# Kernel tuning notes

Hardware: AMD Instinct MI355X
Metric: run time of the kernel (lower is better)

Reference implementation:

```python
import jax, jax.numpy as jnp
import numpy as np

EPS_BN = 1e-5


def conv2d(x, w, b, stride=1, pad=0):
    y = jax.lax.conv_general_dilated(
        x, w, (stride, stride), [(pad, pad), (pad, pad)],
        dimension_numbers=('NCHW', 'OIHW', 'NCHW'))
    return y + b[None, :, None, None]


def resize_ac(x, oh, ow):
    # bilinear resize, align_corners=True (matches F.interpolate(..., align_corners=True))
    N, C, H, W = x.shape
    ys = jnp.linspace(0.0, H - 1.0, oh)
    xs = jnp.linspace(0.0, W - 1.0, ow)
    y0 = jnp.floor(ys).astype(jnp.int32)
    x0 = jnp.floor(xs).astype(jnp.int32)
    y1 = jnp.minimum(y0 + 1, H - 1)
    x1 = jnp.minimum(x0 + 1, W - 1)
    wy = (ys - y0)[None, None, :, None]
    wx = (xs - x0)[None, None, None, :]
    top = jnp.take(x, y0, axis=2)
    bot = jnp.take(x, y1, axis=2)
    rows = top * (1.0 - wy) + bot * wy
    left = jnp.take(rows, x0, axis=3)
    right = jnp.take(rows, x1, axis=3)
    return left * (1.0 - wx) + right * wx


def grid_sample_3d(vol, grid):
    # vol: (N,C,D,H,W); grid: (N,Do,Ho,Wo,3) with channels (x->W, y->H, z->D)
    # trilinear, padding_mode='zeros', align_corners=False (torch defaults)
    N, C, D, H, W = vol.shape
    out_shape = grid.shape[1:4]
    gx = grid[..., 0].reshape(N, -1)
    gy = grid[..., 1].reshape(N, -1)
    gz = grid[..., 2].reshape(N, -1)
    ix = ((gx + 1.0) * W - 1.0) * 0.5
    iy = ((gy + 1.0) * H - 1.0) * 0.5
    iz = ((gz + 1.0) * D - 1.0) * 0.5
    x0 = jnp.floor(ix); y0 = jnp.floor(iy); z0 = jnp.floor(iz)
    fx = ix - x0; fy = iy - y0; fz = iz - z0
    volf = vol.reshape(N, C, D * H * W)

    def corner(xi, yi, zi, wgt):
        valid = ((xi >= 0) & (xi < W) & (yi >= 0) & (yi < H) & (zi >= 0) & (zi < D))
        xc = jnp.clip(xi, 0, W - 1).astype(jnp.int32)
        yc = jnp.clip(yi, 0, H - 1).astype(jnp.int32)
        zc = jnp.clip(zi, 0, D - 1).astype(jnp.int32)
        lin = (zc * H + yc) * W + xc  # (N,P)
        g = jnp.take_along_axis(volf, lin[:, None, :], axis=2)  # (N,C,P)
        return g * (wgt * valid.astype(vol.dtype))[:, None, :]

    out = 0.0
    for zi, wz in ((z0, 1.0 - fz), (z0 + 1.0, fz)):
        for yi, wy in ((y0, 1.0 - fy), (y0 + 1.0, fy)):
            for xi, wx in ((x0, 1.0 - fx), (x0 + 1.0, fx)):
                out = out + corner(xi, yi, zi, wz * wy * wx)
    return out.reshape(N, C, *out_shape)


def setup_inputs() -> dict:
    key = jax.random.key(0)
    ks = jax.random.split(key, 9)
    N, H, W = 1, 2048, 2048
    f = lambda k, shp, s: jax.random.normal(k, shp, jnp.float32) * s
    return dict(
        low=jax.random.uniform(ks[0], (N, 3, H, W), jnp.float32),
        med=jax.random.uniform(ks[1], (N, 3, H, W), jnp.float32),
        high=jax.random.uniform(ks[2], (N, 3, H, W), jnp.float32),
        w1=f(ks[3], (16, 9, 3, 3), 0.1), b1=jnp.zeros((16,), jnp.float32),
        w2=f(ks[4], (32, 16, 3, 3), 0.1), b2=jnp.zeros((32,), jnp.float32),
        w3=f(ks[5], (64, 32, 3, 3), 0.1), b3=jnp.zeros((64,), jnp.float32),
        w4=f(ks[6], (192, 64, 1, 1), 0.1), b4=jnp.zeros((192,), jnp.float32),
        gw1=f(ks[7], (16, 3, 1, 1), 0.3), gb1=jnp.zeros((16,), jnp.float32),
        g_gamma=jnp.ones((16,), jnp.float32), g_beta=jnp.zeros((16,), jnp.float32),
        g_mean=jnp.zeros((16,), jnp.float32), g_var=jnp.ones((16,), jnp.float32),
        gw2=f(ks[8], (1, 16, 1, 1), 0.3), gb2=jnp.zeros((1,), jnp.float32),
    )


def _forward(low, med, high, w1, b1, w2, b2, w3, b3, w4, b4,
             gw1, gb1, g_gamma, g_beta, g_mean, g_var, gw2, gb2):
    img = 0.33 * low + 0.33 * med + 0.33 * high  # (N,3,H,W)

    # ---- Coeffs: downsample 9-ch input to 128x128, run coeff net -> (N,12,16,16,16)
    x = resize_ac(jnp.concatenate([low, med, high], axis=1), 128, 128)
    x = jax.nn.relu(conv2d(x, w1, b1, stride=2, pad=1))   # 64x64
    x = jax.nn.relu(conv2d(x, w2, b2, stride=2, pad=1))   # 32x32
    x = jax.nn.relu(conv2d(x, w3, b3, stride=2, pad=1))   # 16x16
    coeff = conv2d(x, w4, b4, stride=1, pad=0)            # (N,192,16,16)
    grid_vol = coeff.reshape(-1, 12, 16, 16, 16)          # (N,12,D,H,W)

    # ---- GuideNN at full res: 1x1 conv -> BN(eval) -> ReLU -> 1x1 conv -> sigmoid
    g = conv2d(img, gw1, gb1)
    g = g_gamma[None, :, None, None] * (g - g_mean[None, :, None, None]) \
        * jax.lax.rsqrt(g_var[None, :, None, None] + EPS_BN) + g_beta[None, :, None, None]
    g = jax.nn.relu(g)
    guide = jax.nn.sigmoid(conv2d(g, gw2, gb2))           # (N,1,H,W)
    guide = resize_ac(guide, 64, 64)[:, 0]                # (N,64,64)

    # ---- Slice: trilinear lookup into bilateral grid, guided by (guide, hg, wg)
    N = guide.shape[0]
    lin = (jnp.arange(64, dtype=jnp.float32) / 63.0) * 2.0 - 1.0
    hg = jnp.broadcast_to(lin[:, None], (64, 64))
    wg = jnp.broadcast_to(lin[None, :], (64, 64))
    grid = jnp.stack([guide,
                      jnp.broadcast_to(hg, guide.shape),
                      jnp.broadcast_to(wg, guide.shape)], axis=-1)[:, None]  # (N,1,64,64,3)
    sc = grid_sample_3d(grid_vol, grid)[:, :, 0]          # (N,12,64,64)

    # ---- Apply: upsample coeffs to full res, per-pixel 3x4 affine (HDRNet apply)
    Hi, Wi = img.shape[2], img.shape[3]
    cf = resize_ac(sc, Hi, Wi).reshape(N, 3, 4, Hi, Wi)
    out = jnp.einsum('ncjhw,njhw->nchw', cf[:, :, :3], img) + cf[:, :, 3]
    return out


def reference(low, med, high, w1, b1, w2, b2, w3, b3, w4, b4,
              gw1, gb1, g_gamma, g_beta, g_mean, g_var, gw2, gb2):
    return _forward(low, med, high, w1, b1, w2, b2, w3, b3, w4, b4,
                    gw1, gb1, g_gamma, g_beta, g_mean, g_var, gw2, gb2)
```

## Files before the change

### kernel.cpp

```cpp
#include <hip/hip_runtime.h>
#include <math.h>

#define HH 2048
#define WW 2048
#define HWFULL (HH*WW)

typedef float v4f __attribute__((ext_vector_type(4)));
union F4 { float4 v; v4f c; float f[4]; };

__global__ __launch_bounds__(256) void k_ds9_guide(
        const float* __restrict__ low, const float* __restrict__ med,
        const float* __restrict__ high,
        const float* __restrict__ gw1, const float* __restrict__ gb1,
        const float* __restrict__ gamma, const float* __restrict__ beta,
        const float* __restrict__ mean, const float* __restrict__ var,
        const float* __restrict__ gw2, const float* __restrict__ gb2,
        float* __restrict__ ds9, float* __restrict__ guideb) {
    int idx = blockIdx.x * 256 + threadIdx.x;
    if (idx < 147456) {
        int ch = idx >> 14;
        int rem = idx & 16383;
        int oy = rem >> 7, ox = rem & 127;
        const float* base = (ch < 3) ? low : (ch < 6 ? med : high);
        const float* p = base + (ch % 3) * HWFULL;
        float ysf = oy * (2047.0f / 127.0f);
        int y0 = (int)ysf; if (y0 > 2047) y0 = 2047;
        int y1 = y0 + 1;   if (y1 > 2047) y1 = 2047;
        float wy = ysf - (float)y0;
        float xsf = ox * (2047.0f / 127.0f);
        int x0 = (int)xsf; if (x0 > 2047) x0 = 2047;
        int x1 = x0 + 1;   if (x1 > 2047) x1 = 2047;
        float wx = xsf - (float)x0;
        float t = p[y0 * WW + x0] * (1.0f - wx) + p[y0 * WW + x1] * wx;
        float b = p[y1 * WW + x0] * (1.0f - wx) + p[y1 * WW + x1] * wx;
        ds9[idx] = t * (1.0f - wy) + b * wy;
    } else {
        int g = idx - 147456;
        int h = g >> 6, w = g & 63;
        float ysf = h * (2047.0f / 63.0f);
        int y0 = (int)ysf; if (y0 > 2047) y0 = 2047;
        int y1 = y0 + 1;   if (y1 > 2047) y1 = 2047;
        float wy = ysf - (float)y0;
        float xsf = w * (2047.0f / 63.0f);
        int x0 = (int)xsf; if (x0 > 2047) x0 = 2047;
        int x1 = x0 + 1;   if (x1 > 2047) x1 = 2047;
        float wx = xsf - (float)x0;
        int yy[2] = { y0, y1 };
        int xx[2] = { x0, x1 };
        float gp[2][2];
        #pragma unroll
        for (int a = 0; a < 2; ++a) {
            #pragma unroll
            for (int bb = 0; bb < 2; ++bb) {
                int pix = yy[a] * WW + xx[bb];
                float i0 = 0.33f * (low[pix]            + med[pix]            + high[pix]);
                float i1 = 0.33f * (low[HWFULL + pix]   + med[HWFULL + pix]   + high[HWFULL + pix]);
                float i2 = 0.33f * (low[2*HWFULL + pix] + med[2*HWFULL + pix] + high[2*HWFULL + pix]);
                float acc = gb2[0];
                for (int k = 0; k < 16; ++k) {
                    float t = gb1[k] + gw1[k*3] * i0 + gw1[k*3+1] * i1 + gw1[k*3+2] * i2;
                    t = gamma[k] * (t - mean[k]) * (1.0f / sqrtf(var[k] + 1e-5f)) + beta[k];
                    t = fmaxf(t, 0.0f);
                    acc += gw2[k] * t;
                }
                gp[a][bb] = 1.0f / (1.0f + expf(-acc));
            }
        }
        guideb[g] = (1.0f - wy) * ((1.0f - wx) * gp[0][0] + wx * gp[0][1])
                  +         wy  * ((1.0f - wx) * gp[1][0] + wx * gp[1][1]);
    }
}

__global__ __launch_bounds__(256) void k_conv1(const float* __restrict__ in,
                                               const float* __restrict__ w,
                                               const float* __restrict__ b,
                                               float* __restrict__ out) {
    __shared__ float sd[9 * 3 * 34];
    const int oy = blockIdx.x >> 2;
    const int q  = blockIdx.x & 3;
    const int tid = threadIdx.x;
    for (int idx = tid; idx < 9 * 3 * 33; idx += 256) {
        int ch = idx / 99;
        int rem = idx - 99 * ch;
        int r = rem / 33;
        int j = rem - 33 * r;
        int x = 32 * q - 1 + j;
        int iy = 2 * oy - 1 + r;
        sd[(ch * 3 + r) * 34 + j] =
            (x >= 0 && x < 128 && iy >= 0 && iy < 128) ? in[ch * 16384 + iy * 128 + x] : 0.0f;
    }
    __syncthreads();
    int co = tid >> 4, xl = tid & 15;
    float acc = b[co];
    for (int ci = 0; ci < 9; ++ci) {
        #pragma unroll
        for (int ky = 0; ky < 3; ++ky) {
            const float* wr = w + ((co * 9 + ci) * 3 + ky) * 3;
            const float* row = &sd[(ci * 3 + ky) * 34 + 2 * xl];
            acc += wr[0] * row[0] + wr[1] * row[1] + wr[2] * row[2];
        }
    }
    out[co * 4096 + oy * 64 + 16 * q + xl] = fmaxf(acc, 0.0f);
}

__global__ __launch_bounds__(256) void k_conv2(const float* __restrict__ in,
                                               const float* __restrict__ w,
                                               const float* __restrict__ b,
                                               float* __restrict__ out) {
    __shared__ float sd[16 * 3 * 18];
    const int oy = blockIdx.x >> 2;
    const int q  = blockIdx.x & 3;
    const int tid = threadIdx.x;
    for (int idx = tid; idx < 16 * 3 * 17; idx += 256) {
        int ch = idx / 51;
        int rem = idx - 51 * ch;
        int r = rem / 17;
        int j = rem - 17 * r;
        int x = 16 * q - 1 + j;
        int iy = 2 * oy - 1 + r;
        sd[(ch * 3 + r) * 18 + j] =
            (x >= 0 && x < 64 && iy >= 0 && iy < 64) ? in[ch * 4096 + iy * 64 + x] : 0.0f;
    }
    __syncthreads();
    int co = tid >> 3, xl = tid & 7;
    float acc = b[co];
    for (int ci = 0; ci < 16; ++ci) {
        #pragma unroll
        for (int ky = 0; ky < 3; ++ky) {
            const float* wr = w + ((co * 16 + ci) * 3 + ky) * 3;
            const float* row = &sd[(ci * 3 + ky) * 18 + 2 * xl];
            acc += wr[0] * row[0] + wr[1] * row[1] + wr[2] * row[2];
        }
    }
    out[co * 1024 + oy * 32 + 8 * q + xl] = fmaxf(acc, 0.0f);
}

__global__ __launch_bounds__(256) void k_conv34(const float* __restrict__ in,
                                                const float* __restrict__ w3,
                                                const float* __restrict__ b3,
                                                const float* __restrict__ w4,
                                                const float* __restrict__ b4,
                                                float* __restrict__ gridvol) {
    __shared__ float sd[32 * 3 * 10];
    __shared__ float sc3[64 * 4];
    const int oy = blockIdx.x >> 2;
    const int q  = blockIdx.x & 3;
    const int tid = threadIdx.x;
    for (int idx = tid; idx < 32 * 3 * 9; idx += 256) {
        int ch = idx / 27;
        int rem = idx - 27 * ch;
        int r = rem / 9;
        int j = rem - 9 * r;
        int x = 8 * q - 1 + j;
        int iy = 2 * oy - 1 + r;
        sd[(ch * 3 + r) * 10 + j] =
            (x >= 0 && x < 32 && iy >= 0 && iy < 32) ? in[ch * 1024 + iy * 32 + x] : 0.0f;
    }
    __syncthreads();
    {
        int co = tid >> 2, xl = tid & 3;
        float acc = b3[co];
        for (int ci = 0; ci < 32; ++ci) {
            #pragma unroll
            for (int ky = 0; ky < 3; ++ky) {
                const float* wr = w3 + ((co * 32 + ci) * 3 + ky) * 3;
                const float* row = &sd[(ci * 3 + ky) * 10 + 2 * xl];
                acc += wr[0] * row[0] + wr[1] * row[1] + wr[2] * row[2];
            }
        }
        sc3[co * 4 + xl] = fmaxf(acc, 0.0f);
    }
    __syncthreads();
    {
        int px = tid & 3;
        int ob = tid >> 2;
        #pragma unroll
        for (int k = 0; k < 3; ++k) {
            int o = ob + 64 * k;
            float sum = b4[o];
            const float* wp = w4 + o * 64;
            for (int i = 0; i < 64; ++i)
                sum += wp[i] * sc3[i * 4 + px];
            gridvol[o * 256 + oy * 16 + 4 * q + px] = sum;
        }
    }
}

__global__ __launch_bounds__(256) void k_slice_ab(
        const float* __restrict__ gridvol, const float* __restrict__ guideb,
        float* __restrict__ ab_full) {
    __shared__ float s[3 * 64 * 12];
    const int b = blockIdx.x;
    const int tid = threadIdx.x;
    float byf = (8 * b) * (63.0f / 2047.0f);
    int v0 = (int)byf; if (v0 > 63) v0 = 63;

    if (tid < 192) {
        int rr = tid >> 6, x = tid & 63;
        int srow = v0 + rr; if (srow > 63) srow = 63;
        float guide = guideb[srow * 64 + x];
        float hg = srow * (2.0f / 63.0f) - 1.0f;
        float wg = x * (2.0f / 63.0f) - 1.0f;
        float ix = ((guide + 1.0f) * 16.0f - 1.0f) * 0.5f;
        float iy = ((hg    + 1.0f) * 16.0f - 1.0f) * 0.5f;
        float iz = ((wg    + 1.0f) * 16.0f - 1.0f) * 0.5f;
        float xf = floorf(ix), yf = floorf(iy), zf = floorf(iz);
        float fx = ix - xf, fyy = iy - yf, fz = iz - zf;
        int xi = (int)xf, yi = (int)yf, zi = (int)zf;
        float scv[12];
        #pragma unroll
        for (int c = 0; c < 12; ++c) scv[c] = 0.0f;
        #pragma unroll
        for (int dz = 0; dz < 2; ++dz) {
            int z = zi + dz; float wz = dz ? fz : 1.0f - fz;
            if (z < 0 || z > 15) continue;
            #pragma unroll
            for (int dy = 0; dy < 2; ++dy) {
                int yv = yi + dy; float wyv = dy ? fyy : 1.0f - fyy;
                if (yv < 0 || yv > 15) continue;
                #pragma unroll
                for (int dx = 0; dx < 2; ++dx) {
                    int xv = xi + dx; float wxv = dx ? fx : 1.0f - fx;
                    if (xv < 0 || xv > 15) continue;
                    float wgt = wz * wyv * wxv;
                    int base = yv * 16 + xv;
                    #pragma unroll
                    for (int c = 0; c < 12; ++c)
                        scv[c] += wgt * gridvol[(c * 16 + z) * 256 + base];
                }
            }
        }
        #pragma unroll
        for (int c = 0; c < 12; ++c) s[(rr * 64 + x) * 12 + c] = scv[c];
    }
    __syncthreads();

    #pragma unroll
    for (int k = 0; k < 24; ++k) {
        int e = k * 256 + tid;
        int r8 = e / 768;
        int rem = e - 768 * r8;
        int x = rem / 12;
        int c = rem - 12 * x;
        int y = 8 * b + r8;
        float iyf = y * (63.0f / 2047.0f);
        int y0 = (int)iyf; if (y0 > 63) y0 = 63;
        int y1 = y0 + 1;   if (y1 > 63) y1 = 63;
        float fy = iyf - (float)y0;
        int i0 = y0 - v0, i1 = y1 - v0;
        float t = s[(i0 * 64 + x) * 12 + c];
        float bo = s[(i1 * 64 + x) * 12 + c];
        ab_full[y * 768 + rem] = t + (bo - t) * fy;
    }
}

__global__ __launch_bounds__(256) void k_apply(
        const float* __restrict__ low, const float* __restrict__ med,
        const float* __restrict__ high, const float* __restrict__ ab_full,
        float* __restrict__ out) {
    __shared__ F4 abs4[192];
    const int y = blockIdx.x >> 1;
    const int half = blockIdx.x & 1;
    const int tid = threadIdx.x;
    const int v = half * 256 + tid;
    const int vi = (y << 9) + v;
    const int HW4 = HWFULL / 4;

    const float4* Lp = (const float4*)low;
    const float4* Mp = (const float4*)med;
    const float4* Hp = (const float4*)high;
    F4 l0, l1, l2, m0, m1, m2, h0, h1, h2;
    l0.v = Lp[vi]; l1.v = Lp[vi + HW4]; l2.v = Lp[vi + 2 * HW4];
    m0.v = Mp[vi]; m1.v = Mp[vi + HW4]; m2.v = Mp[vi + 2 * HW4];
    h0.v = Hp[vi]; h1.v = Hp[vi + HW4]; h2.v = Hp[vi + 2 * HW4];

    if (tid < 192)
        abs4[tid].v = ((const float4*)(ab_full + y * 768))[tid];
    __syncthreads();

    int x_first = v << 2;
    float ixf0 = x_first * (63.0f / 2047.0f);
    int f = (int)ixf0; if (f > 63) f = 63;
    float ixf3 = (x_first + 3) * (63.0f / 2047.0f);
    int s3 = (int)ixf3; if (s3 > 63) s3 = 63;
    int fp1 = f + 1;  if (fp1 > 63) fp1 = 63;
    int sp1 = s3 + 1; if (sp1 > 63) sp1 = 63;
    F4 A0[3], B0[3], C0[3];
    #pragma unroll
    for (int qq = 0; qq < 3; ++qq) {
        A0[qq] = abs4[f   * 3 + qq];
        B0[qq] = abs4[fp1 * 3 + qq];
        C0[qq] = abs4[sp1 * 3 + qq];
    }

    F4 o0, o1, o2;
    #pragma unroll
    for (int p = 0; p < 4; ++p) {
        int x = x_first + p;
        float ixf = x * (63.0f / 2047.0f);
        int x0 = (int)ixf; if (x0 > 63) x0 = 63;
        float fx = ixf - (float)x0;
        bool first = (x0 == f);
        float im0 = 0.33f * (l0.f[p] + m0.f[p] + h0.f[p]);
        float im1 = 0.33f * (l1.f[p] + m1.f[p] + h1.f[p]);
        float im2 = 0.33f * (l2.f[p] + m2.f[p] + h2.f[p]);
        float cf[12];
        #pragma unroll
        for (int qq = 0; qq < 3; ++qq) {
            #pragma unroll
            for (int r = 0; r < 4; ++r) {
                float a = first ? A0[qq].f[r] : B0[qq].f[r];
                float bb = first ? B0[qq].f[r] : C0[qq].f[r];
                cf[qq * 4 + r] = a + (bb - a) * fx;
            }
        }
        o0.f[p] = cf[0] * im0 + cf[1]  * im1 + cf[2]  * im2 + cf[3];
        o1.f[p] = cf[4] * im0 + cf[5]  * im1 + cf[6]  * im2 + cf[7];
        o2.f[p] = cf[8] * im0 + cf[9]  * im1 + cf[10] * im2 + cf[11];
    }
    v4f* Op = (v4f*)out;
    __builtin_nontemporal_store(o0.c, &Op[vi]);
    __builtin_nontemporal_store(o1.c, &Op[vi + HW4]);
    __builtin_nontemporal_store(o2.c, &Op[vi + 2 * HW4]);
}

extern "C" void kernel_launch(void* const* d_in, const int* in_sizes, int n_in,
                              void* d_out, int out_size, void* d_ws, size_t ws_size,
                              hipStream_t stream) {
    const float* low   = (const float*)d_in[0];
    const float* med   = (const float*)d_in[1];
    const float* high  = (const float*)d_in[2];
    const float* w1    = (const float*)d_in[3];
    const float* b1    = (const float*)d_in[4];
    const float* w2    = (const float*)d_in[5];
    const float* b2    = (const float*)d_in[6];
    const float* w3    = (const float*)d_in[7];
    const float* b3    = (const float*)d_in[8];
    const float* w4    = (const float*)d_in[9];
    const float* b4    = (const float*)d_in[10];
    const float* gw1   = (const float*)d_in[11];
    const float* gb1   = (const float*)d_in[12];
    const float* gamma = (const float*)d_in[13];
    const float* beta  = (const float*)d_in[14];
    const float* mean  = (const float*)d_in[15];
    const float* var   = (const float*)d_in[16];
    const float* gw2   = (const float*)d_in[17];
    const float* gb2   = (const float*)d_in[18];
    float* out = (float*)d_out;

    float* ws      = (float*)d_ws;
    float* ab_full = ws;
    float* ds9     = ab_full + 1572864;
    float* c1      = ds9 + 147456;
    float* c2v     = c1 + 65536;
    float* gridvol = c2v + 32768;
    float* guideb  = gridvol + 49152;

    hipLaunchKernelGGL(k_ds9_guide, dim3(592), dim3(256), 0, stream,
                       low, med, high, gw1, gb1, gamma, beta, mean, var, gw2, gb2,
                       ds9, guideb);
    hipLaunchKernelGGL(k_conv1,    dim3(256), dim3(256), 0, stream, ds9, w1, b1, c1);
    hipLaunchKernelGGL(k_conv2,    dim3(128), dim3(256), 0, stream, c1, w2, b2, c2v);
    hipLaunchKernelGGL(k_conv34,   dim3(64),  dim3(256), 0, stream, c2v, w3, b3, w4, b4, gridvol);
    hipLaunchKernelGGL(k_slice_ab, dim3(256), dim3(256), 0, stream, gridvol, guideb, ab_full);
    hipLaunchKernelGGL(k_apply,    dim3(4096), dim3(256), 0, stream, low, med, high, ab_full, out);
}
```

Baseline: 84.52 us.

## Fuse downsample into conv1, guide into conv2, drop LDS staging in apply

Removes the separate downsample-and-guide kernel. The bilinear downsample is now computed inline while conv1 loads its shared-memory tile, and the guide MLP moves into conv2's spare threads. This drops one launch and the ds9 round trip through global memory. In apply, the per-row coefficient staging in LDS and the barrier are gone, coefficients are read straight from global (cached) memory, and the nontemporal stores become plain stores. In exchange, conv1 recomputes halo samples it shares with neighbouring blocks, and only 32 threads per conv2 block do the serial guide work.

After: 81.20 us. -3.9%, faster.

```diff
diff --git a/kernel.cpp b/kernel.cpp
--- a/kernel.cpp
+++ b/kernel.cpp
@@ -8,70 +8,9 @@
 typedef float v4f __attribute__((ext_vector_type(4)));
 union F4 { float4 v; v4f c; float f[4]; };
 
-__global__ __launch_bounds__(256) void k_ds9_guide(
-        const float* __restrict__ low, const float* __restrict__ med,
-        const float* __restrict__ high,
-        const float* __restrict__ gw1, const float* __restrict__ gb1,
-        const float* __restrict__ gamma, const float* __restrict__ beta,
-        const float* __restrict__ mean, const float* __restrict__ var,
-        const float* __restrict__ gw2, const float* __restrict__ gb2,
-        float* __restrict__ ds9, float* __restrict__ guideb) {
-    int idx = blockIdx.x * 256 + threadIdx.x;
-    if (idx < 147456) {
-        int ch = idx >> 14;
-        int rem = idx & 16383;
-        int oy = rem >> 7, ox = rem & 127;
-        const float* base = (ch < 3) ? low : (ch < 6 ? med : high);
-        const float* p = base + (ch % 3) * HWFULL;
-        float ysf = oy * (2047.0f / 127.0f);
-        int y0 = (int)ysf; if (y0 > 2047) y0 = 2047;
-        int y1 = y0 + 1;   if (y1 > 2047) y1 = 2047;
-        float wy = ysf - (float)y0;
-        float xsf = ox * (2047.0f / 127.0f);
-        int x0 = (int)xsf; if (x0 > 2047) x0 = 2047;
-        int x1 = x0 + 1;   if (x1 > 2047) x1 = 2047;
-        float wx = xsf - (float)x0;
-        float t = p[y0 * WW + x0] * (1.0f - wx) + p[y0 * WW + x1] * wx;
-        float b = p[y1 * WW + x0] * (1.0f - wx) + p[y1 * WW + x1] * wx;
-        ds9[idx] = t * (1.0f - wy) + b * wy;
-    } else {
-        int g = idx - 147456;
-        int h = g >> 6, w = g & 63;
-        float ysf = h * (2047.0f / 63.0f);
-        int y0 = (int)ysf; if (y0 > 2047) y0 = 2047;
-        int y1 = y0 + 1;   if (y1 > 2047) y1 = 2047;
-        float wy = ysf - (float)y0;
-        float xsf = w * (2047.0f / 63.0f);
-        int x0 = (int)xsf; if (x0 > 2047) x0 = 2047;
-        int x1 = x0 + 1;   if (x1 > 2047) x1 = 2047;
-        float wx = xsf - (float)x0;
-        int yy[2] = { y0, y1 };
-        int xx[2] = { x0, x1 };
-        float gp[2][2];
-        #pragma unroll
-        for (int a = 0; a < 2; ++a) {
-            #pragma unroll
-            for (int bb = 0; bb < 2; ++bb) {
-                int pix = yy[a] * WW + xx[bb];
-                float i0 = 0.33f * (low[pix]            + med[pix]            + high[pix]);
-                float i1 = 0.33f * (low[HWFULL + pix]   + med[HWFULL + pix]   + high[HWFULL + pix]);
-                float i2 = 0.33f * (low[2*HWFULL + pix] + med[2*HWFULL + pix] + high[2*HWFULL + pix]);
-                float acc = gb2[0];
-                for (int k = 0; k < 16; ++k) {
-                    float t = gb1[k] + gw1[k*3] * i0 + gw1[k*3+1] * i1 + gw1[k*3+2] * i2;
-                    t = gamma[k] * (t - mean[k]) * (1.0f / sqrtf(var[k] + 1e-5f)) + beta[k];
-                    t = fmaxf(t, 0.0f);
-                    acc += gw2[k] * t;
-                }
-                gp[a][bb] = 1.0f / (1.0f + expf(-acc));
-            }
-        }
-        guideb[g] = (1.0f - wy) * ((1.0f - wx) * gp[0][0] + wx * gp[0][1])
-                  +         wy  * ((1.0f - wx) * gp[1][0] + wx * gp[1][1]);
-    }
-}
-
-__global__ __launch_bounds__(256) void k_conv1(const float* __restrict__ in,
+__global__ __launch_bounds__(256) void k_conv1(const float* __restrict__ low,
+                                               const float* __restrict__ med,
+                                               const float* __restrict__ high,
                                                const float* __restrict__ w,
                                                const float* __restrict__ b,
                                                float* __restrict__ out) {
@@ -84,10 +23,25 @@
         int rem = idx - 99 * ch;
         int r = rem / 33;
         int j = rem - 33 * r;
-        int x = 32 * q - 1 + j;
-        int iy = 2 * oy - 1 + r;
-        sd[(ch * 3 + r) * 34 + j] =
-            (x >= 0 && x < 128 && iy >= 0 && iy < 128) ? in[ch * 16384 + iy * 128 + x] : 0.0f;
+        int ix128 = 32 * q - 1 + j;
+        int iy128 = 2 * oy - 1 + r;
+        float val = 0.0f;
+        if (ix128 >= 0 && ix128 < 128 && iy128 >= 0 && iy128 < 128) {
+            const float* base = (ch < 3) ? low : (ch < 6 ? med : high);
+            const float* p = base + (ch % 3) * HWFULL;
+            float ysf = iy128 * (2047.0f / 127.0f);
+            int y0 = (int)ysf; if (y0 > 2047) y0 = 2047;
+            int y1 = y0 + 1;   if (y1 > 2047) y1 = 2047;
+            float wy = ysf - (float)y0;
+            float xsf = ix128 * (2047.0f / 127.0f);
+            int x0 = (int)xsf; if (x0 > 2047) x0 = 2047;
+            int x1 = x0 + 1;   if (x1 > 2047) x1 = 2047;
+            float wx = xsf - (float)x0;
+            float t = p[y0 * WW + x0] * (1.0f - wx) + p[y0 * WW + x1] * wx;
+            float bo = p[y1 * WW + x0] * (1.0f - wx) + p[y1 * WW + x1] * wx;
+            val = t * (1.0f - wy) + bo * wy;
+        }
+        sd[(ch * 3 + r) * 34 + j] = val;
     }
     __syncthreads();
     int co = tid >> 4, xl = tid & 15;
@@ -106,7 +60,15 @@
 __global__ __launch_bounds__(256) void k_conv2(const float* __restrict__ in,
                                                const float* __restrict__ w,
                                                const float* __restrict__ b,
-                                               float* __restrict__ out) {
+                                               const float* __restrict__ low,
+                                               const float* __restrict__ med,
+                                               const float* __restrict__ high,
+                                               const float* __restrict__ gw1, const float* __restrict__ gb1,
+                                               const float* __restrict__ gamma, const float* __restrict__ beta,
+                                               const float* __restrict__ mean, const float* __restrict__ var,
+                                               const float* __restrict__ gw2, const float* __restrict__ gb2,
+                                               float* __restrict__ out,
+                                               float* __restrict__ guideb) {
     __shared__ float sd[16 * 3 * 18];
     const int oy = blockIdx.x >> 2;
     const int q  = blockIdx.x & 3;
@@ -133,6 +95,42 @@
         }
     }
     out[co * 1024 + oy * 32 + 8 * q + xl] = fmaxf(acc, 0.0f);
+
+    if (tid < 32) {
+        int g = blockIdx.x * 32 + tid;
+        int h = g >> 6, wv = g & 63;
+        float ysf = h * (2047.0f / 63.0f);
+        int y0 = (int)ysf; if (y0 > 2047) y0 = 2047;
+        int y1 = y0 + 1;   if (y1 > 2047) y1 = 2047;
+        float wy = ysf - (float)y0;
+        float xsf = wv * (2047.0f / 63.0f);
+        int x0 = (int)xsf; if (x0 > 2047) x0 = 2047;
+        int x1 = x0 + 1;   if (x1 > 2047) x1 = 2047;
+        float wx = xsf - (float)x0;
+        int yy[2] = { y0, y1 };
+        int xx[2] = { x0, x1 };
+        float gp[2][2];
+        #pragma unroll
+        for (int a = 0; a < 2; ++a) {
+            #pragma unroll
+            for (int bb = 0; bb < 2; ++bb) {
+                int pix = yy[a] * WW + xx[bb];
+                float i0 = 0.33f * (low[pix]            + med[pix]            + high[pix]);
+                float i1 = 0.33f * (low[HWFULL + pix]   + med[HWFULL + pix]   + high[HWFULL + pix]);
+                float i2 = 0.33f * (low[2*HWFULL + pix] + med[2*HWFULL + pix] + high[2*HWFULL + pix]);
+                float acc2 = gb2[0];
+                for (int k = 0; k < 16; ++k) {
+                    float t = gb1[k] + gw1[k*3] * i0 + gw1[k*3+1] * i1 + gw1[k*3+2] * i2;
+                    t = gamma[k] * (t - mean[k]) * (1.0f / sqrtf(var[k] + 1e-5f)) + beta[k];
+                    t = fmaxf(t, 0.0f);
+                    acc2 += gw2[k] * t;
+                }
+                gp[a][bb] = 1.0f / (1.0f + expf(-acc2));
+            }
+        }
+        guideb[g] = (1.0f - wy) * ((1.0f - wx) * gp[0][0] + wx * gp[0][1])
+                  +         wy  * ((1.0f - wx) * gp[1][0] + wx * gp[1][1]);
+    }
 }
 
 __global__ __launch_bounds__(256) void k_conv34(const float* __restrict__ in,
@@ -258,26 +256,21 @@
         const float* __restrict__ low, const float* __restrict__ med,
         const float* __restrict__ high, const float* __restrict__ ab_full,
         float* __restrict__ out) {
-    __shared__ F4 abs4[192];
-    const int y = blockIdx.x >> 1;
-    const int half = blockIdx.x & 1;
-    const int tid = threadIdx.x;
-    const int v = half * 256 + tid;
-    const int vi = (y << 9) + v;
+    const int g = blockIdx.x * 256 + threadIdx.x;
+    const int y = g >> 9;
+    const int v = g & 511;
     const int HW4 = HWFULL / 4;
 
     const float4* Lp = (const float4*)low;
     const float4* Mp = (const float4*)med;
     const float4* Hp = (const float4*)high;
+
     F4 l0, l1, l2, m0, m1, m2, h0, h1, h2;
-    l0.v = Lp[vi]; l1.v = Lp[vi + HW4]; l2.v = Lp[vi + 2 * HW4];
-    m0.v = Mp[vi]; m1.v = Mp[vi + HW4]; m2.v = Mp[vi + 2 * HW4];
-    h0.v = Hp[vi]; h1.v = Hp[vi + HW4]; h2.v = Hp[vi + 2 * HW4];
-
-    if (tid < 192)
-        abs4[tid].v = ((const float4*)(ab_full + y * 768))[tid];
-    __syncthreads();
-
+    l0.v = Lp[g]; l1.v = Lp[g + HW4]; l2.v = Lp[g + 2 * HW4];
+    m0.v = Mp[g]; m1.v = Mp[g + HW4]; m2.v = Mp[g + 2 * HW4];
+    h0.v = Hp[g]; h1.v = Hp[g + HW4]; h2.v = Hp[g + 2 * HW4];
+
+    const float4* abr = (const float4*)(ab_full + y * 768);
     int x_first = v << 2;
     float ixf0 = x_first * (63.0f / 2047.0f);
     int f = (int)ixf0; if (f > 63) f = 63;
@@ -288,9 +281,9 @@
     F4 A0[3], B0[3], C0[3];
     #pragma unroll
     for (int qq = 0; qq < 3; ++qq) {
-        A0[qq] = abs4[f   * 3 + qq];
-        B0[qq] = abs4[fp1 * 3 + qq];
-        C0[qq] = abs4[sp1 * 3 + qq];
+        A0[qq].v = abr[f   * 3 + qq];
+        B0[qq].v = abr[fp1 * 3 + qq];
+        C0[qq].v = abr[sp1 * 3 + qq];
     }
 
     F4 o0, o1, o2;
@@ -318,10 +311,10 @@
         o1.f[p] = cf[4] * im0 + cf[5]  * im1 + cf[6]  * im2 + cf[7];
         o2.f[p] = cf[8] * im0 + cf[9]  * im1 + cf[10] * im2 + cf[11];
     }
-    v4f* Op = (v4f*)out;
-    __builtin_nontemporal_store(o0.c, &Op[vi]);
-    __builtin_nontemporal_store(o1.c, &Op[vi + HW4]);
-    __builtin_nontemporal_store(o2.c, &Op[vi + 2 * HW4]);
+    float4* Op = (float4*)out;
+    Op[g]           = o0.v;
+    Op[g + HW4]     = o1.v;
+    Op[g + 2 * HW4] = o2.v;
 }
 
 extern "C" void kernel_launch(void* const* d_in, const int* in_sizes, int n_in,
@@ -350,17 +343,16 @@
 
     float* ws      = (float*)d_ws;
     float* ab_full = ws;
-    float* ds9     = ab_full + 1572864;
-    float* c1      = ds9 + 147456;
+    float* c1      = ab_full + 1572864;
     float* c2v     = c1 + 65536;
     float* gridvol = c2v + 32768;
     float* guideb  = gridvol + 49152;
 
-    hipLaunchKernelGGL(k_ds9_guide, dim3(592), dim3(256), 0, stream,
-                       low, med, high, gw1, gb1, gamma, beta, mean, var, gw2, gb2,
-                       ds9, guideb);
-    hipLaunchKernelGGL(k_conv1,    dim3(256), dim3(256), 0, stream, ds9, w1, b1, c1);
-    hipLaunchKernelGGL(k_conv2,    dim3(128), dim3(256), 0, stream, c1, w2, b2, c2v);
+    hipLaunchKernelGGL(k_conv1,    dim3(256), dim3(256), 0, stream,
+                       low, med, high, w1, b1, c1);
+    hipLaunchKernelGGL(k_conv2,    dim3(128), dim3(256), 0, stream,
+                       c1, w2, b2, low, med, high,
+                       gw1, gb1, gamma, beta, mean, var, gw2, gb2, c2v, guideb);
     hipLaunchKernelGGL(k_conv34,   dim3(64),  dim3(256), 0, stream, c2v, w3, b3, w4, b4, gridvol);
     hipLaunchKernelGGL(k_slice_ab, dim3(256), dim3(256), 0, stream, gridvol, guideb, ab_full);
     hipLaunchKernelGGL(k_apply,    dim3(4096), dim3(256), 0, stream, low, med, high, ab_full, out);
```
